# Kernel optimization log

Measured on AMD Instinct MI355X. Metric: run time of the kernel, lower is better.

## Reference

```python
import jax, jax.numpy as jnp
import numpy as np

CH = 64
SCALE = 2
GROUPS = 4
K = 3
GN_GROUPS = min(CH // 8, 8)  # = 8
EPS_GN = 1e-5
EPS_COS = 1e-8


def setup_inputs() -> dict:
    key = jax.random.key(0)
    ks = jax.random.split(key, 4)
    B, H, W = 8, 256, 256
    OC = 2 * GROUPS
    lap = jnp.array([[0., -1., 0.], [-1., 4., -1.], [0., -1., 0.]], dtype=jnp.float32)
    hp_weight = jnp.tile(lap[None, None], (CH, 1, 1, 1))  # depthwise high-pass kernel
    return {
        "x": jax.random.normal(ks[0], (B, CH, H, W), dtype=jnp.float32),
        "gn_gamma": jnp.ones((CH,), jnp.float32),
        "gn_beta": jnp.zeros((CH,), jnp.float32),
        "hp_weight": hp_weight,
        "dir_w": jax.random.normal(ks[1], (OC, K * K - 1), jnp.float32) * 0.001,
        "dir_b": jnp.zeros((OC,), jnp.float32),
        "mag_w": jax.random.normal(ks[2], (OC, CH), jnp.float32) * 0.02,
        "mag_b": jnp.zeros((OC,), jnp.float32),
        "hfg_w": jax.random.normal(ks[3], (OC, CH), jnp.float32) * 0.02,
        "hfg_b": jnp.zeros((OC,), jnp.float32),
    }


def group_norm(x, gamma, beta, g, eps=EPS_GN):
    B, C, H, W = x.shape
    xr = x.reshape(B, g, -1)
    mu = xr.mean(-1, keepdims=True)
    var = xr.var(-1, keepdims=True)
    xn = ((xr - mu) * jax.lax.rsqrt(var + eps)).reshape(B, C, H, W)
    return xn * gamma[None, :, None, None] + beta[None, :, None, None]


def dw_conv3(x, w):
    # depthwise 3x3, padding=1, no bias
    return jax.lax.conv_general_dilated(
        x, w, window_strides=(1, 1), padding=((1, 1), (1, 1)),
        dimension_numbers=("NCHW", "OIHW", "NCHW"), feature_group_count=x.shape[1])


def avg_pool(x, s):
    B, C, H, W = x.shape
    return x.reshape(B, C, H // s, s, W // s, s).mean(axis=(3, 5))


def direction_feat(x, k=K):
    # cosine similarity (over channels) of center pixel vs each of k*k neighbors, center dropped
    B, C, H, W = x.shape
    p = k // 2
    xp = jnp.pad(x, ((0, 0), (0, 0), (p, p), (p, p)))
    patches = jnp.stack([xp[:, :, i:i + H, j:j + W]
                         for i in range(k) for j in range(k)], axis=2)  # [B,C,k2,H,W]
    center = patches[:, :, k * k // 2:k * k // 2 + 1]  # [B,C,1,H,W]
    dot = (center * patches).sum(axis=1)               # [B,k2,H,W]
    n1 = jnp.sqrt((center * center).sum(axis=1))       # [B,1,H,W]
    n2 = jnp.sqrt((patches * patches).sum(axis=1))     # [B,k2,H,W]
    sim = dot / (jnp.maximum(n1, EPS_COS) * jnp.maximum(n2, EPS_COS))
    c = k * k // 2
    return jnp.concatenate([sim[:, :c], sim[:, c + 1:]], axis=1)  # [B,k2-1,H,W]


def conv1x1(w, b, x):
    return jnp.einsum("oc,bchw->bohw", w, x) + b[None, :, None, None]


def grid_sample_border(x, grid):
    # x: [N,C,H,W]; grid: [N,Hg,Wg,2] in [-1,1]; bilinear, align_corners=False, padding_mode='border'
    N, C, H, W = x.shape
    gx, gy = grid[..., 0], grid[..., 1]
    ix = jnp.clip(((gx + 1.0) * W - 1.0) * 0.5, 0.0, W - 1.0)
    iy = jnp.clip(((gy + 1.0) * H - 1.0) * 0.5, 0.0, H - 1.0)
    x0 = jnp.floor(ix); y0 = jnp.floor(iy)
    wx = (ix - x0)[..., None]; wy = (iy - y0)[..., None]
    x0i = jnp.clip(x0.astype(jnp.int32), 0, W - 1)
    y0i = jnp.clip(y0.astype(jnp.int32), 0, H - 1)
    x1i = jnp.clip(x0i + 1, 0, W - 1)
    y1i = jnp.clip(y0i + 1, 0, H - 1)
    img = x.transpose(0, 2, 3, 1)  # [N,H,W,C]
    b = jnp.arange(N)[:, None, None]
    v00 = img[b, y0i, x0i]; v01 = img[b, y0i, x1i]
    v10 = img[b, y1i, x0i]; v11 = img[b, y1i, x1i]
    out = (v00 * (1 - wx) * (1 - wy) + v01 * wx * (1 - wy)
           + v10 * (1 - wx) * wy + v11 * wx * wy)
    return out.transpose(0, 3, 1, 2)  # [N,C,Hg,Wg]


def reference(x, gn_gamma, gn_beta, hp_weight, dir_w, dir_b, mag_w, mag_b, hfg_w, hfg_b):
    B, C, H, W = x.shape
    xn = group_norm(x, gn_gamma, gn_beta, GN_GROUPS)
    hf = dw_conv3(xn, hp_weight)
    xl = avg_pool(xn, SCALE)
    hfl = avg_pool(hf, SCALE)
    df = direction_feat(xl)
    gate = jax.nn.sigmoid(conv1x1(mag_w, mag_b, xl) + conv1x1(hfg_w, hfg_b, hfl))
    offset = conv1x1(dir_w, dir_b, df) * gate  # [B, 2*GROUPS, Hl, Wl]
    Hl, Wl = H // SCALE, W // SCALE
    off = offset.reshape(B, 2, GROUPS, Hl, Wl)
    cy = jnp.arange(Hl, dtype=x.dtype) * SCALE + SCALE / 2.0  # high-res pixel centers
    cx = jnp.arange(Wl, dtype=x.dtype) * SCALE + SCALE / 2.0
    gx = (cx[None, None, None, :] + off[:, 0]) * (2.0 / W) - 1.0  # [B,G,Hl,Wl]
    gy = (cy[None, None, :, None] + off[:, 1]) * (2.0 / H) - 1.0
    grid = jnp.stack([gx, gy], axis=-1).reshape(B * GROUPS, Hl, Wl, 2)
    xg = x.reshape(B * GROUPS, C // GROUPS, H, W)
    out = grid_sample_border(xg, grid)
    return out.reshape(B, C, Hl, Wl)
```

## Files before the change

### kernel.cpp

```cpp
#include <hip/hip_runtime.h>
#include <hip/hip_bf16.h>
#include <math.h>

#define B_ 8
#define C_ 64
#define H_ 256
#define W_ 256
#define HL_ 128
#define WL_ 128
#define GN_G 8
#define CPG 8
#define GRP 4
#define OC_ 8
#define GROUP_ELEMS (CPG * H_ * W_)

#define TILE_H 16
#define XROWS 34
#define EOW 132

__device__ __forceinline__ float bf2f(unsigned short u) {
  return __uint_as_float(((unsigned)u) << 16);
}

__global__ __launch_bounds__(256) void k2_fused(const float* __restrict__ x,
                                                const float* __restrict__ hpw,
                                                __hip_bfloat16* __restrict__ px,
                                                __hip_bfloat16* __restrict__ pL,
                                                float* __restrict__ partials) {
  __shared__ float E[XROWS][EOW];
  __shared__ float O[XROWS][EOW];
  __shared__ float rs[4], rs2[4];
  const int t = threadIdx.x;
  const int blk = blockIdx.x;
  const int tileIdx = blk & 7;
  const int bc = blk >> 3;
  const int c = bc & 63;
  const int hl0 = tileIdx * TILE_H;
  const float* plane = x + (size_t)bc * (H_ * W_);
  const int y0 = 2 * hl0 - 1;

  if (t < XROWS * 2) {
    const int r = t >> 1;
    if (t & 1) E[r][128] = 0.f; else O[r][0] = 0.f;
  }

  float s = 0.f, s2 = 0.f;
  for (int i = 0; i < 9; ++i) {
    const int q = t + i * 256;
    if (q >= XROWS * 64) break;
    const int r = q >> 6;
    const int k = q & 63;
    const int y = y0 + r;
    float4 v = make_float4(0.f, 0.f, 0.f, 0.f);
    if ((unsigned)y < (unsigned)H_)
      v = *reinterpret_cast<const float4*>(plane + y * W_ + (k << 2));
    E[r][2 * k]     = v.x;
    E[r][2 * k + 1] = v.z;
    O[r][2 * k + 1] = v.y;
    O[r][2 * k + 2] = v.w;
    if (r >= 1 && r <= 32) {
      s  += v.x + v.y + v.z + v.w;
      s2 += v.x * v.x + v.y * v.y + v.z * v.z + v.w * v.w;
    }
  }
#pragma unroll
  for (int off = 32; off > 0; off >>= 1) {
    s  += __shfl_down(s, off, 64);
    s2 += __shfl_down(s2, off, 64);
  }
  if ((t & 63) == 0) { rs[t >> 6] = s; rs2[t >> 6] = s2; }
  __syncthreads();
  if (t == 0) {
    partials[blk * 2 + 0] = rs[0] + rs[1] + rs[2] + rs[3];
    partials[blk * 2 + 1] = rs2[0] + rs2[1] + rs2[2] + rs2[3];
  }

  float w[9];
#pragma unroll
  for (int i = 0; i < 9; ++i) w[i] = hpw[c * 9 + i];

  const int wl = t & 127;
  const int hs = (t >> 7) * 8;
  const int rbase = 2 * hs;
  float win[4][4];
#pragma unroll
  for (int j = 0; j < 4; ++j) {
    win[j][0] = O[rbase + j][wl];
    win[j][1] = E[rbase + j][wl];
    win[j][2] = O[rbase + j][wl + 1];
    win[j][3] = E[rbase + j][wl + 1];
  }

  int outIdx = (bc * HL_ + (hl0 + hs)) * WL_ + wl;
#pragma unroll
  for (int i = 0; i < 8; ++i) {
    float pr[4][3];
#pragma unroll
    for (int j = 0; j < 4; ++j)
#pragma unroll
      for (int d = 0; d < 3; ++d) pr[j][d] = win[j][d] + win[j][d + 1];
    float hfsum = 0.f;
    float q11 = 0.f;
#pragma unroll
    for (int j = 0; j < 3; ++j)
#pragma unroll
      for (int d = 0; d < 3; ++d) {
        const float qq = pr[j][d] + pr[j + 1][d];
        hfsum = fmaf(w[j * 3 + d], qq, hfsum);
        if (j == 1 && d == 1) q11 = qq;
      }
    px[outIdx] = __float2bfloat16(0.25f * q11);
    pL[outIdx] = __float2bfloat16(0.25f * hfsum);
    outIdx += WL_;
    if (i < 7) {
      const int rn = rbase + 2 * i + 4;
#pragma unroll
      for (int d = 0; d < 4; ++d) {
        win[0][d] = win[2][d];
        win[1][d] = win[3][d];
      }
      win[2][0] = O[rn][wl];     win[2][1] = E[rn][wl];
      win[2][2] = O[rn][wl + 1]; win[2][3] = E[rn][wl + 1];
      win[3][0] = O[rn + 1][wl];     win[3][1] = E[rn + 1][wl];
      win[3][2] = O[rn + 1][wl + 1]; win[3][3] = E[rn + 1][wl + 1];
    }
  }
}

__global__ __launch_bounds__(512) void k1_finish(const float* __restrict__ partials,
                                                 const float* __restrict__ gamma,
                                                 const float* __restrict__ beta,
                                                 float* __restrict__ ab) {
  const int t = threadIdx.x;
  const int b = t >> 6, c = t & 63, g = c >> 3;
  float S = 0.f, S2 = 0.f;
  for (int c2 = g * CPG; c2 < g * CPG + CPG; ++c2)
#pragma unroll
    for (int p = 0; p < 8; ++p) {
      const int blk = (b * 64 + c2) * 8 + p;
      S  += partials[blk * 2 + 0];
      S2 += partials[blk * 2 + 1];
    }
  const float N = (float)GROUP_ELEMS;
  const float mean = S / N;
  const float var = fmaxf(S2 / N - mean * mean, 0.f);
  const float a = rsqrtf(var + 1e-5f) * gamma[c];
  ab[t * 2 + 0] = a;
  ab[t * 2 + 1] = beta[c] - mean * a;
}

#define TS 16
__global__ __launch_bounds__(256) void k34_fused(const float* __restrict__ x,
                                                 const __hip_bfloat16* __restrict__ px,
                                                 const __hip_bfloat16* __restrict__ pL,
                                                 const float* __restrict__ ab,
                                                 const float* __restrict__ dir_w,
                                                 const float* __restrict__ dir_b,
                                                 const float* __restrict__ mag_w,
                                                 const float* __restrict__ mag_b,
                                                 const float* __restrict__ hfg_w,
                                                 const float* __restrict__ hfg_b,
                                                 float* __restrict__ out) {
  __shared__ float s_v[16][18][24];
  __shared__ float s_mw[C_][OC_];
  __shared__ float s_hw[C_][OC_];
  __shared__ float s_dir[OC_][8];
  __shared__ float s_ab2[C_][2];
  __shared__ float s_bias[2][OC_];

  const int tid = threadIdx.x;
  const int bx = blockIdx.x;
  const int tx = bx & 7, ty = (bx >> 3) & 7, b = bx >> 6;
  const int hl0 = ty * TS, wl0 = tx * TS;
  const size_t planeSz = (size_t)HL_ * WL_;

  for (int i = tid; i < OC_ * C_; i += 256) {
    const int o = i >> 6, c = i & 63;
    s_mw[c][o] = mag_w[i];
    s_hw[c][o] = hfg_w[i];
  }
  if (tid < 64) s_dir[tid >> 3][tid & 7] = dir_w[tid];
  if (tid < 128) s_ab2[tid >> 1][tid & 1] = ab[b * 128 + tid];
  if (tid < OC_) { s_bias[0][tid] = mag_b[tid] + hfg_b[tid]; s_bias[1][tid] = dir_b[tid]; }

  const int pxi = tid & 15, pyi = tid >> 4;
  const int hl = hl0 + pyi, wl = wl0 + pxi;
  const float mterm = 0.5f * ((hl == 0) + (hl == HL_ - 1) + (wl == 0) + (wl == WL_ - 1));

  float dot[8], n2[8], z[8], n1 = 0.f;
#pragma unroll
  for (int k = 0; k < 8; ++k) { dot[k] = 0.f; n2[k] = 0.f; z[k] = 0.f; }

  for (int cc = 0; cc < 4; ++cc) {
    float lh[16];
    {
      const unsigned short* lp = reinterpret_cast<const unsigned short*>(
          pL + (size_t)(b * C_ + cc * 16) * planeSz + hl * WL_ + wl);
#pragma unroll
      for (int c = 0; c < 16; ++c) lh[c] = bf2f(lp[c * planeSz]);
    }

    __syncthreads();

    for (int q = tid; q < 16 * 18 * 6; q += 256) {
      const int c = q / 108, rem = q % 108, r = rem / 6, f4 = rem % 6;
      const int cg = cc * 16 + c;
      const int gy = hl0 - 1 + r;
      const int gx0 = wl0 - 4 + f4 * 4;
      const float a = s_ab2[cg][0], bb = s_ab2[cg][1];
      const __hip_bfloat16* pp = px + (size_t)(b * C_ + cg) * planeSz + gy * WL_ + gx0;
      float4 v = make_float4(0.f, 0.f, 0.f, 0.f);
      if ((unsigned)gy < (unsigned)HL_) {
        if (gx0 >= 0 && gx0 + 3 < WL_) {
          const ushort4 rv = *reinterpret_cast<const ushort4*>(pp);
          v.x = fmaf(a, bf2f(rv.x), bb); v.y = fmaf(a, bf2f(rv.y), bb);
          v.z = fmaf(a, bf2f(rv.z), bb); v.w = fmaf(a, bf2f(rv.w), bb);
        } else {
          const unsigned short* ps = reinterpret_cast<const unsigned short*>(pp);
          if ((unsigned)(gx0 + 0) < (unsigned)WL_) v.x = fmaf(a, bf2f(ps[0]), bb);
          if ((unsigned)(gx0 + 1) < (unsigned)WL_) v.y = fmaf(a, bf2f(ps[1]), bb);
          if ((unsigned)(gx0 + 2) < (unsigned)WL_) v.z = fmaf(a, bf2f(ps[2]), bb);
          if ((unsigned)(gx0 + 3) < (unsigned)WL_) v.w = fmaf(a, bf2f(ps[3]), bb);
        }
      }
      *reinterpret_cast<float4*>(&s_v[c][r][f4 * 4]) = v;
    }
    __syncthreads();

#pragma unroll
    for (int c = 0; c < 16; ++c) {
      const int cg = cc * 16 + c;
      const float a = s_ab2[cg][0], bb = s_ab2[cg][1];
      const float vc = s_v[c][pyi + 1][pxi + 4];
      const float vh = fmaf(a, lh[c], bb * mterm);
      n1 = fmaf(vc, vc, n1);
      const float u0 = s_v[c][pyi][pxi + 3];
      const float u1 = s_v[c][pyi][pxi + 4];
      const float u2 = s_v[c][pyi][pxi + 5];
      const float u3 = s_v[c][pyi + 1][pxi + 3];
      const float u4 = s_v[c][pyi + 1][pxi + 5];
      const float u5 = s_v[c][pyi + 2][pxi + 3];
      const float u6 = s_v[c][pyi + 2][pxi + 4];
      const float u7 = s_v[c][pyi + 2][pxi + 5];
      dot[0] = fmaf(vc, u0, dot[0]); n2[0] = fmaf(u0, u0, n2[0]);
      dot[1] = fmaf(vc, u1, dot[1]); n2[1] = fmaf(u1, u1, n2[1]);
      dot[2] = fmaf(vc, u2, dot[2]); n2[2] = fmaf(u2, u2, n2[2]);
      dot[3] = fmaf(vc, u3, dot[3]); n2[3] = fmaf(u3, u3, n2[3]);
      dot[4] = fmaf(vc, u4, dot[4]); n2[4] = fmaf(u4, u4, n2[4]);
      dot[5] = fmaf(vc, u5, dot[5]); n2[5] = fmaf(u5, u5, n2[5]);
      dot[6] = fmaf(vc, u6, dot[6]); n2[6] = fmaf(u6, u6, n2[6]);
      dot[7] = fmaf(vc, u7, dot[7]); n2[7] = fmaf(u7, u7, n2[7]);
      const float4 mw0 = *reinterpret_cast<const float4*>(&s_mw[cg][0]);
      const float4 mw1 = *reinterpret_cast<const float4*>(&s_mw[cg][4]);
      const float4 hw0 = *reinterpret_cast<const float4*>(&s_hw[cg][0]);
      const float4 hw1 = *reinterpret_cast<const float4*>(&s_hw[cg][4]);
      z[0] = fmaf(mw0.x, vc, fmaf(hw0.x, vh, z[0]));
      z[1] = fmaf(mw0.y, vc, fmaf(hw0.y, vh, z[1]));
      z[2] = fmaf(mw0.z, vc, fmaf(hw0.z, vh, z[2]));
      z[3] = fmaf(mw0.w, vc, fmaf(hw0.w, vh, z[3]));
      z[4] = fmaf(mw1.x, vc, fmaf(hw1.x, vh, z[4]));
      z[5] = fmaf(mw1.y, vc, fmaf(hw1.y, vh, z[5]));
      z[6] = fmaf(mw1.z, vc, fmaf(hw1.z, vh, z[6]));
      z[7] = fmaf(mw1.w, vc, fmaf(hw1.w, vh, z[7]));
    }
  }

  const float n1c = fmaxf(sqrtf(n1), 1e-8f);
  float df[8];
#pragma unroll
  for (int k = 0; k < 8; ++k)
    df[k] = dot[k] / (n1c * fmaxf(sqrtf(n2[k]), 1e-8f));

  float off[8];
#pragma unroll
  for (int o = 0; o < 8; ++o) {
    float t1 = s_bias[1][o];
#pragma unroll
    for (int j = 0; j < 8; ++j) t1 = fmaf(s_dir[o][j], df[j], t1);
    const float zz = z[o] + s_bias[0][o];
    off[o] = t1 / (1.f + expf(-zz));
  }

  const float* planeB = x + (size_t)(b * C_) * (H_ * W_);
  float* outB = out + (size_t)(b * C_) * planeSz + hl * WL_ + wl;
#pragma unroll
  for (int g = 0; g < GRP; ++g) {
    const float ix = fminf(fmaxf(2.f * wl + 0.5f + off[g], 0.f), (float)(W_ - 1));
    const float iy = fminf(fmaxf(2.f * hl + 0.5f + off[GRP + g], 0.f), (float)(H_ - 1));
    const float x0f = floorf(ix), y0f = floorf(iy);
    const float wx = ix - x0f, wy = iy - y0f;
    const int x0 = (int)x0f, y0 = (int)y0f;
    const float w00 = (1.f - wx) * (1.f - wy), w01 = wx * (1.f - wy);
    const float w10 = (1.f - wx) * wy,        w11 = wx * wy;
    const float* pc = planeB + (size_t)(g * 16) * (H_ * W_);
    float* oc = outB + (size_t)(g * 16) * planeSz;
    if (__builtin_expect(((x0 | y0) & 1) == 0, 1)) {
#pragma unroll 4
      for (int c2 = 0; c2 < 16; ++c2) {
        const float2 r0 = *reinterpret_cast<const float2*>(pc + y0 * W_ + x0);
        const float2 r1 = *reinterpret_cast<const float2*>(pc + (y0 + 1) * W_ + x0);
        *oc = fmaf(r0.x, w00, fmaf(r0.y, w01, fmaf(r1.x, w10, r1.y * w11)));
        pc += H_ * W_;
        oc += planeSz;
      }
    } else {
      const int x1 = min(x0 + 1, W_ - 1), y1 = min(y0 + 1, H_ - 1);
#pragma unroll 4
      for (int c2 = 0; c2 < 16; ++c2) {
        const float v00 = pc[y0 * W_ + x0];
        const float v01 = pc[y0 * W_ + x1];
        const float v10 = pc[y1 * W_ + x0];
        const float v11 = pc[y1 * W_ + x1];
        *oc = fmaf(v00, w00, fmaf(v01, w01, fmaf(v10, w10, v11 * w11)));
        pc += H_ * W_;
        oc += planeSz;
      }
    }
  }
}

extern "C" void kernel_launch(void* const* d_in, const int* in_sizes, int n_in,
                              void* d_out, int out_size, void* d_ws, size_t ws_size,
                              hipStream_t stream) {
  const float* x = (const float*)d_in[0];
  const float* gn_gamma = (const float*)d_in[1];
  const float* gn_beta = (const float*)d_in[2];
  const float* hp_weight = (const float*)d_in[3];
  const float* dir_w = (const float*)d_in[4];
  const float* dir_b = (const float*)d_in[5];
  const float* mag_w = (const float*)d_in[6];
  const float* mag_b = (const float*)d_in[7];
  const float* hfg_w = (const float*)d_in[8];
  const float* hfg_b = (const float*)d_in[9];
  float* out = (float*)d_out;

  float* ws = (float*)d_ws;
  float* partials = ws;
  float* ab = ws + 8192;
  __hip_bfloat16* px = (__hip_bfloat16*)(ws + 16384);
  __hip_bfloat16* pL = px + (size_t)B_ * C_ * HL_ * WL_;

  k2_fused<<<B_ * C_ * 8, 256, 0, stream>>>(x, hp_weight, px, pL, partials);
  k1_finish<<<1, 512, 0, stream>>>(partials, gn_gamma, gn_beta, ab);
  k34_fused<<<B_ * (HL_ / TS) * (WL_ / TS), 256, 0, stream>>>(x, px, pL, ab, dir_w, dir_b,
                                                              mag_w, mag_b, hfg_w, hfg_b, out);
}
```

Measured before the change: 94.84 us.

## Gather from bf16 copy of x and fold GroupNorm finish into sampler

The first kernel now also writes a bf16 copy of the input, and the grid-sample gather reads that copy instead of the fp32 input. This halves the bytes fetched by the gather. The separate GroupNorm statistics kernel is removed, and each sampling block now reduces the partial sums itself. This costs an extra 64MB write and lowers the precision of the sampled values. The bf16 path is used only when the workspace is large enough.

Measured after the change: 98.09 us. 3.4% more time.

```diff
diff --git a/kernel.cpp b/kernel.cpp
--- a/kernel.cpp
+++ b/kernel.cpp
@@ -21,11 +21,17 @@
 __device__ __forceinline__ float bf2f(unsigned short u) {
   return __uint_as_float(((unsigned)u) << 16);
 }
-
+__device__ __forceinline__ unsigned short f2bfbits(float f) {
+  __hip_bfloat16 h = __float2bfloat16(f);
+  return *reinterpret_cast<unsigned short*>(&h);
+}
+
+template <int USE_XB>
 __global__ __launch_bounds__(256) void k2_fused(const float* __restrict__ x,
                                                 const float* __restrict__ hpw,
                                                 __hip_bfloat16* __restrict__ px,
                                                 __hip_bfloat16* __restrict__ pL,
+                                                unsigned short* __restrict__ xb,
                                                 float* __restrict__ partials) {
   __shared__ float E[XROWS][EOW];
   __shared__ float O[XROWS][EOW];
@@ -61,6 +67,12 @@
     if (r >= 1 && r <= 32) {
       s  += v.x + v.y + v.z + v.w;
       s2 += v.x * v.x + v.y * v.y + v.z * v.z + v.w * v.w;
+      if (USE_XB) {
+        ushort4 bv;
+        bv.x = f2bfbits(v.x); bv.y = f2bfbits(v.y);
+        bv.z = f2bfbits(v.z); bv.w = f2bfbits(v.w);
+        *reinterpret_cast<ushort4*>(xb + (size_t)bc * (H_ * W_) + y * W_ + (k << 2)) = bv;
+      }
     }
   }
 #pragma unroll
@@ -127,33 +139,15 @@
   }
 }
 
-__global__ __launch_bounds__(512) void k1_finish(const float* __restrict__ partials,
+#define TS 16
+template <int USE_XB>
+__global__ __launch_bounds__(256) void k34_fused(const float* __restrict__ x,
+                                                 const unsigned short* __restrict__ xb,
+                                                 const __hip_bfloat16* __restrict__ px,
+                                                 const __hip_bfloat16* __restrict__ pL,
+                                                 const float* __restrict__ partials,
                                                  const float* __restrict__ gamma,
                                                  const float* __restrict__ beta,
-                                                 float* __restrict__ ab) {
-  const int t = threadIdx.x;
-  const int b = t >> 6, c = t & 63, g = c >> 3;
-  float S = 0.f, S2 = 0.f;
-  for (int c2 = g * CPG; c2 < g * CPG + CPG; ++c2)
-#pragma unroll
-    for (int p = 0; p < 8; ++p) {
-      const int blk = (b * 64 + c2) * 8 + p;
-      S  += partials[blk * 2 + 0];
-      S2 += partials[blk * 2 + 1];
-    }
-  const float N = (float)GROUP_ELEMS;
-  const float mean = S / N;
-  const float var = fmaxf(S2 / N - mean * mean, 0.f);
-  const float a = rsqrtf(var + 1e-5f) * gamma[c];
-  ab[t * 2 + 0] = a;
-  ab[t * 2 + 1] = beta[c] - mean * a;
-}
-
-#define TS 16
-__global__ __launch_bounds__(256) void k34_fused(const float* __restrict__ x,
-                                                 const __hip_bfloat16* __restrict__ px,
-                                                 const __hip_bfloat16* __restrict__ pL,
-                                                 const float* __restrict__ ab,
                                                  const float* __restrict__ dir_w,
                                                  const float* __restrict__ dir_b,
                                                  const float* __restrict__ mag_w,
@@ -180,8 +174,24 @@
     s_hw[c][o] = hfg_w[i];
   }
   if (tid < 64) s_dir[tid >> 3][tid & 7] = dir_w[tid];
-  if (tid < 128) s_ab2[tid >> 1][tid & 1] = ab[b * 128 + tid];
   if (tid < OC_) { s_bias[0][tid] = mag_b[tid] + hfg_b[tid]; s_bias[1][tid] = dir_b[tid]; }
+  if (tid < 64) {
+    const int c = tid, g = c >> 3;
+    float S = 0.f, S2 = 0.f;
+    for (int c2 = g * CPG; c2 < g * CPG + CPG; ++c2)
+#pragma unroll
+      for (int p2 = 0; p2 < 8; ++p2) {
+        const int blk2 = (b * 64 + c2) * 8 + p2;
+        S  += partials[blk2 * 2 + 0];
+        S2 += partials[blk2 * 2 + 1];
+      }
+    const float N = (float)GROUP_ELEMS;
+    const float mean = S / N;
+    const float var = fmaxf(S2 / N - mean * mean, 0.f);
+    const float a = rsqrtf(var + 1e-5f) * gamma[c];
+    s_ab2[c][0] = a;
+    s_ab2[c][1] = beta[c] - mean * a;
+  }
 
   const int pxi = tid & 15, pyi = tid >> 4;
   const int hl = hl0 + pyi, wl = wl0 + pxi;
@@ -281,7 +291,6 @@
     off[o] = t1 / (1.f + expf(-zz));
   }
 
-  const float* planeB = x + (size_t)(b * C_) * (H_ * W_);
   float* outB = out + (size_t)(b * C_) * planeSz + hl * WL_ + wl;
 #pragma unroll
   for (int g = 0; g < GRP; ++g) {
@@ -292,28 +301,55 @@
     const int x0 = (int)x0f, y0 = (int)y0f;
     const float w00 = (1.f - wx) * (1.f - wy), w01 = wx * (1.f - wy);
     const float w10 = (1.f - wx) * wy,        w11 = wx * wy;
-    const float* pc = planeB + (size_t)(g * 16) * (H_ * W_);
     float* oc = outB + (size_t)(g * 16) * planeSz;
-    if (__builtin_expect(((x0 | y0) & 1) == 0, 1)) {
+    if (USE_XB) {
+      const unsigned short* pc = xb + (size_t)(b * C_ + g * 16) * (H_ * W_);
+      if (__builtin_expect(((x0 | y0) & 1) == 0, 1)) {
 #pragma unroll 4
-      for (int c2 = 0; c2 < 16; ++c2) {
-        const float2 r0 = *reinterpret_cast<const float2*>(pc + y0 * W_ + x0);
-        const float2 r1 = *reinterpret_cast<const float2*>(pc + (y0 + 1) * W_ + x0);
-        *oc = fmaf(r0.x, w00, fmaf(r0.y, w01, fmaf(r1.x, w10, r1.y * w11)));
-        pc += H_ * W_;
-        oc += planeSz;
+        for (int c2 = 0; c2 < 16; ++c2) {
+          const ushort2 r0 = *reinterpret_cast<const ushort2*>(pc + y0 * W_ + x0);
+          const ushort2 r1 = *reinterpret_cast<const ushort2*>(pc + (y0 + 1) * W_ + x0);
+          *oc = fmaf(bf2f(r0.x), w00, fmaf(bf2f(r0.y), w01,
+                fmaf(bf2f(r1.x), w10, bf2f(r1.y) * w11)));
+          pc += H_ * W_;
+          oc += planeSz;
+        }
+      } else {
+        const int x1 = min(x0 + 1, W_ - 1), y1 = min(y0 + 1, H_ - 1);
+#pragma unroll 4
+        for (int c2 = 0; c2 < 16; ++c2) {
+          const float v00 = bf2f(pc[y0 * W_ + x0]);
+          const float v01 = bf2f(pc[y0 * W_ + x1]);
+          const float v10 = bf2f(pc[y1 * W_ + x0]);
+          const float v11 = bf2f(pc[y1 * W_ + x1]);
+          *oc = fmaf(v00, w00, fmaf(v01, w01, fmaf(v10, w10, v11 * w11)));
+          pc += H_ * W_;
+          oc += planeSz;
+        }
       }
     } else {
-      const int x1 = min(x0 + 1, W_ - 1), y1 = min(y0 + 1, H_ - 1);
+      const float* pc = x + (size_t)(b * C_ + g * 16) * (H_ * W_);
+      if (__builtin_expect(((x0 | y0) & 1) == 0, 1)) {
 #pragma unroll 4
-      for (int c2 = 0; c2 < 16; ++c2) {
-        const float v00 = pc[y0 * W_ + x0];
-        const float v01 = pc[y0 * W_ + x1];
-        const float v10 = pc[y1 * W_ + x0];
-        const float v11 = pc[y1 * W_ + x1];
-        *oc = fmaf(v00, w00, fmaf(v01, w01, fmaf(v10, w10, v11 * w11)));
-        pc += H_ * W_;
-        oc += planeSz;
+        for (int c2 = 0; c2 < 16; ++c2) {
+          const float2 r0 = *reinterpret_cast<const float2*>(pc + y0 * W_ + x0);
+          const float2 r1 = *reinterpret_cast<const float2*>(pc + (y0 + 1) * W_ + x0);
+          *oc = fmaf(r0.x, w00, fmaf(r0.y, w01, fmaf(r1.x, w10, r1.y * w11)));
+          pc += H_ * W_;
+          oc += planeSz;
+        }
+      } else {
+        const int x1 = min(x0 + 1, W_ - 1), y1 = min(y0 + 1, H_ - 1);
+#pragma unroll 4
+        for (int c2 = 0; c2 < 16; ++c2) {
+          const float v00 = pc[y0 * W_ + x0];
+          const float v01 = pc[y0 * W_ + x1];
+          const float v10 = pc[y1 * W_ + x0];
+          const float v11 = pc[y1 * W_ + x1];
+          *oc = fmaf(v00, w00, fmaf(v01, w01, fmaf(v10, w10, v11 * w11)));
+          pc += H_ * W_;
+          oc += planeSz;
+        }
       }
     }
   }
@@ -336,12 +372,22 @@
 
   float* ws = (float*)d_ws;
   float* partials = ws;
-  float* ab = ws + 8192;
-  __hip_bfloat16* px = (__hip_bfloat16*)(ws + 16384);
+  __hip_bfloat16* px = (__hip_bfloat16*)(ws + 8192);
   __hip_bfloat16* pL = px + (size_t)B_ * C_ * HL_ * WL_;
-
-  k2_fused<<<B_ * C_ * 8, 256, 0, stream>>>(x, hp_weight, px, pL, partials);
-  k1_finish<<<1, 512, 0, stream>>>(partials, gn_gamma, gn_beta, ab);
-  k34_fused<<<B_ * (HL_ / TS) * (WL_ / TS), 256, 0, stream>>>(x, px, pL, ab, dir_w, dir_b,
-                                                              mag_w, mag_b, hfg_w, hfg_b, out);
-}
+  unsigned short* xb = (unsigned short*)(pL + (size_t)B_ * C_ * HL_ * WL_);
+
+  const size_t need = 32768 + 2u * 4194304u + 67108864u;
+  const bool use_xb = (ws_size >= need);
+
+  if (use_xb) {
+    k2_fused<1><<<B_ * C_ * 8, 256, 0, stream>>>(x, hp_weight, px, pL, xb, partials);
+    k34_fused<1><<<B_ * (HL_ / TS) * (WL_ / TS), 256, 0, stream>>>(
+        x, xb, px, pL, partials, gn_gamma, gn_beta, dir_w, dir_b,
+        mag_w, mag_b, hfg_w, hfg_b, out);
+  } else {
+    k2_fused<0><<<B_ * C_ * 8, 256, 0, stream>>>(x, hp_weight, px, pL, xb, partials);
+    k34_fused<0><<<B_ * (HL_ / TS) * (WL_ / TS), 256, 0, stream>>>(
+        x, xb, px, pL, partials, gn_gamma, gn_beta, dir_w, dir_b,
+        mag_w, mag_b, hfg_w, hfg_b, out);
+  }
+}
```
